# Kernel optimization log

Hardware: AMD Instinct MI355X
Metric: run time of the kernel (lower is better)

## Reference

```python
import jax, jax.numpy as jnp
import numpy as np

FP8_MAX = 448.0


def _quantize_fp8(x):
    """Per-tensor symmetric quantization matching the Triton kernel's decode.

    Encode: u = round(clip(x*scale, -448, 448) / 448 * 127)  (stored as u+128 in uint8)
    Decode: x_hat = u / 127 * 448 / scale,  with scale = 448 / amax(|x|).
    We keep u as a float array of integers in [-127, 127] (the +128 uint8 bias
    cancels in the kernel's `u - 128`).
    """
    amax = jnp.max(jnp.abs(x))
    scale = FP8_MAX / jnp.maximum(amax, jnp.asarray(1e-12, x.dtype))
    q = jnp.clip(x * scale, -FP8_MAX, FP8_MAX)
    u = jnp.round(q / FP8_MAX * 127.0)
    return u, scale


def reference(x, weight):
    orig_shape = x.shape
    K = weight.shape[1]
    x2d = x.reshape(-1, K)                      # [M, K]

    ua, a_scale = _quantize_fp8(x2d)            # codes + per-tensor scale
    uw, w_scale = _quantize_fp8(weight)         # weight: [N, K]

    # Kernel dequant: val = u / 127 * FP8_MAX; acc in fp32; rescale by 1/(a_scale*b_scale)
    a_f = ua * (FP8_MAX / 127.0)
    b_f = (uw * (FP8_MAX / 127.0)).T            # [K, N] (weight_fp8.t())
    acc = a_f @ b_f                              # fp32 accumulate, [M, N]
    out = acc * (1.0 / (a_scale * w_scale))
    out = out.astype(x.dtype)
    return out.reshape(*orig_shape[:-1], weight.shape[0])


def setup_inputs() -> dict:
    key = jax.random.key(0)
    k1, k2 = jax.random.split(key)
    x = jax.random.normal(k1, (4, 2048, 4096), dtype=jnp.float32)
    weight = jax.random.normal(k2, (8192, 4096), dtype=jnp.float32) * 0.02
    return {"x": x, "weight": weight}
```

## Files before the change

### kernel.cpp

```cpp
#include <hip/hip_runtime.h>

#define FP8_MAX_F 448.0f

static constexpr int M = 8192;
static constexpr int N = 8192;
static constexpr int K = 4096;

typedef __attribute__((ext_vector_type(4))) int i32x4;

__global__ void amax_kernel(const float* __restrict__ x, long n4,
                            unsigned* __restrict__ out) {
    unsigned local = 0u;
    const long stride = (long)gridDim.x * blockDim.x;
    const float4* xv = (const float4*)x;
    for (long i = (long)blockIdx.x * blockDim.x + threadIdx.x; i < n4; i += stride) {
        float4 v = xv[i];
        unsigned a0 = __float_as_uint(v.x) & 0x7fffffffu;
        unsigned a1 = __float_as_uint(v.y) & 0x7fffffffu;
        unsigned a2 = __float_as_uint(v.z) & 0x7fffffffu;
        unsigned a3 = __float_as_uint(v.w) & 0x7fffffffu;
        local = max(local, max(max(a0, a1), max(a2, a3)));
    }
    #pragma unroll
    for (int off = 32; off > 0; off >>= 1)
        local = max(local, (unsigned)__shfl_down((int)local, off, 64));
    __shared__ unsigned smax[4];
    if ((threadIdx.x & 63) == 0) smax[threadIdx.x >> 6] = local;
    __syncthreads();
    if (threadIdx.x == 0) {
        unsigned m01 = max(smax[0], smax[1]);
        unsigned m23 = max(smax[2], smax[3]);
        atomicMax(out, max(m01, m23));
    }
}

__global__ void quant_kernel(const float* __restrict__ x, signed char* __restrict__ q,
                             long n16, const unsigned* __restrict__ amax_bits) {
    const float amax = fmaxf(__uint_as_float(*amax_bits), 1e-12f);
    const float s = FP8_MAX_F / amax;
    const long stride = (long)gridDim.x * blockDim.x;
    const float4* xv = (const float4*)x;
    int4* qv = (int4*)q;
    for (long i = (long)blockIdx.x * blockDim.x + threadIdx.x; i < n16; i += stride) {
        signed char c[16];
        #pragma unroll
        for (int j = 0; j < 4; ++j) {
            float4 v = xv[i * 4 + j];
            float e0 = v.x, e1 = v.y, e2 = v.z, e3 = v.w;
            float f0 = fminf(fmaxf(e0 * s, -FP8_MAX_F), FP8_MAX_F);
            float f1 = fminf(fmaxf(e1 * s, -FP8_MAX_F), FP8_MAX_F);
            float f2 = fminf(fmaxf(e2 * s, -FP8_MAX_F), FP8_MAX_F);
            float f3 = fminf(fmaxf(e3 * s, -FP8_MAX_F), FP8_MAX_F);
            c[j * 4 + 0] = (signed char)(int)rintf(f0 / FP8_MAX_F * 127.0f);
            c[j * 4 + 1] = (signed char)(int)rintf(f1 / FP8_MAX_F * 127.0f);
            c[j * 4 + 2] = (signed char)(int)rintf(f2 / FP8_MAX_F * 127.0f);
            c[j * 4 + 3] = (signed char)(int)rintf(f3 / FP8_MAX_F * 127.0f);
        }
        qv[i] = *(const int4*)c;
    }
}

__global__ __launch_bounds__(256) void gemm_i8_kernel(
    const signed char* __restrict__ A, const signed char* __restrict__ B,
    float* __restrict__ C, const unsigned* __restrict__ amax_bits)
{
    __shared__ signed char a_lds[128 * 64];
    __shared__ signed char b_lds[128 * 64];

    const int tid  = threadIdx.x;
    const int wid  = tid >> 6;
    const int lane = tid & 63;

    const long row0 = (long)blockIdx.x * 128;
    const long col0 = (long)blockIdx.y * 128;

    const int wr = (wid >> 1) * 64;
    const int wc = (wid & 1) * 64;

    i32x4 acc[4][4] = {};

    const int srow = lane >> 2;
    const int scol = (lane & 3) * 16;
    const long a_off = (row0 + wid * 16 + srow) * (long)K + scol;
    const long b_off = (col0 + wid * 16 + srow) * (long)K + scol;
    const signed char* aw0 = A + a_off;
    const signed char* aw1 = A + a_off + 64 * (long)K;
    const signed char* bw0 = B + b_off;
    const signed char* bw1 = B + b_off + 64 * (long)K;

    signed char* a_l0 = &a_lds[wid * 1024];
    signed char* a_l1 = &a_lds[4096 + wid * 1024];
    signed char* b_l0 = &b_lds[wid * 1024];
    signed char* b_l1 = &b_lds[4096 + wid * 1024];

    const int fr = lane & 15;
    const int fq = lane >> 4;

    for (int k0 = 0; k0 < K; k0 += 64) {
        __syncthreads();
        __builtin_amdgcn_global_load_lds(
            (const __attribute__((address_space(1))) void*)(aw0 + k0),
            (__attribute__((address_space(3))) void*)a_l0, 16, 0, 0);
        __builtin_amdgcn_global_load_lds(
            (const __attribute__((address_space(1))) void*)(aw1 + k0),
            (__attribute__((address_space(3))) void*)a_l1, 16, 0, 0);
        __builtin_amdgcn_global_load_lds(
            (const __attribute__((address_space(1))) void*)(bw0 + k0),
            (__attribute__((address_space(3))) void*)b_l0, 16, 0, 0);
        __builtin_amdgcn_global_load_lds(
            (const __attribute__((address_space(1))) void*)(bw1 + k0),
            (__attribute__((address_space(3))) void*)b_l1, 16, 0, 0);
        __syncthreads();

        i32x4 af[4], bf[4];
        #pragma unroll
        for (int mi = 0; mi < 4; ++mi)
            af[mi] = *(const i32x4*)&a_lds[(wr + mi * 16 + fr) * 64 + fq * 16];
        #pragma unroll
        for (int ni = 0; ni < 4; ++ni)
            bf[ni] = *(const i32x4*)&b_lds[(wc + ni * 16 + fr) * 64 + fq * 16];

        #pragma unroll
        for (int mi = 0; mi < 4; ++mi)
            #pragma unroll
            for (int ni = 0; ni < 4; ++ni)
                acc[mi][ni] = __builtin_amdgcn_mfma_i32_16x16x64_i8(
                    af[mi], bf[ni], acc[mi][ni], 0, 0, 0);
    }

    const float amax_x = fmaxf(__uint_as_float(amax_bits[0]), 1e-12f);
    const float amax_w = fmaxf(__uint_as_float(amax_bits[1]), 1e-12f);
    const float factor = amax_x * amax_w * (1.0f / (127.0f * 127.0f));

    #pragma unroll
    for (int mi = 0; mi < 4; ++mi) {
        #pragma unroll
        for (int ni = 0; ni < 4; ++ni) {
            const long col = col0 + wc + ni * 16 + fr;
            #pragma unroll
            for (int j = 0; j < 4; ++j) {
                const long row = row0 + wr + mi * 16 + fq * 4 + j;
                C[row * N + col] = (float)acc[mi][ni][j] * factor;
            }
        }
    }
}

extern "C" void kernel_launch(void* const* d_in, const int* in_sizes, int n_in,
                              void* d_out, int out_size, void* d_ws, size_t ws_size,
                              hipStream_t stream) {
    const float* x = (const float*)d_in[0];
    const float* w = (const float*)d_in[1];
    float* out = (float*)d_out;

    unsigned char* ws = (unsigned char*)d_ws;
    unsigned* amax = (unsigned*)ws;
    signed char* aq = (signed char*)(ws + 256);
    signed char* wq = aq + (long)M * K;

    hipMemsetAsync(amax, 0, 2 * sizeof(unsigned), stream);

    const long nx = (long)M * K;
    const long nw = (long)N * K;
    amax_kernel<<<2048, 256, 0, stream>>>(x, nx / 4, &amax[0]);
    amax_kernel<<<2048, 256, 0, stream>>>(w, nw / 4, &amax[1]);
    quant_kernel<<<2048, 256, 0, stream>>>(x, aq, nx / 16, &amax[0]);
    quant_kernel<<<2048, 256, 0, stream>>>(w, wq, nw / 16, &amax[1]);

    dim3 grid(M / 128, N / 128);
    gemm_i8_kernel<<<grid, 256, 0, stream>>>(aq, wq, out, amax);
}
```

Before: 507.3 us.

## Rewrite int8 GEMM with 256x256 tiles, 4-stage LDS pipeline, swizzled layout

The GEMM moves from 128x128 tiles with 4 waves to 256x256 tiles with 8 waves. It uses a four-buffer LDS ring that prefetches two k-steps ahead with direct global-to-LDS loads, and interleaves MFMA phases with s_setprio and explicit barriers. The quantize kernel now writes data in an XOR-swizzled layout that matches the LDS read pattern, to avoid bank conflicts. The amax and quantize kernels for x and weight are each merged into a single launch. In exchange it uses 128KB of LDS per block and many more accumulator registers, with a risk of register spilling or low occupancy.

```diff
diff --git a/kernel.cpp b/kernel.cpp
--- a/kernel.cpp
+++ b/kernel.cpp
@@ -8,138 +8,191 @@
 
 typedef __attribute__((ext_vector_type(4))) int i32x4;
 
-__global__ void amax_kernel(const float* __restrict__ x, long n4,
+#define AS1 __attribute__((address_space(1)))
+#define AS3 __attribute__((address_space(3)))
+#define BARRIER() asm volatile("s_barrier" ::: "memory")
+#define VMCNT(n)  asm volatile("s_waitcnt vmcnt(" #n ")" ::: "memory")
+
+__global__ void amax_kernel(const float* __restrict__ x, const float* __restrict__ w,
                             unsigned* __restrict__ out) {
-    unsigned local = 0u;
+    const long n4x = (long)M * K / 4;
+    const long n4t = n4x + (long)N * K / 4;
+    unsigned lx = 0u, lw = 0u;
     const long stride = (long)gridDim.x * blockDim.x;
-    const float4* xv = (const float4*)x;
-    for (long i = (long)blockIdx.x * blockDim.x + threadIdx.x; i < n4; i += stride) {
-        float4 v = xv[i];
-        unsigned a0 = __float_as_uint(v.x) & 0x7fffffffu;
-        unsigned a1 = __float_as_uint(v.y) & 0x7fffffffu;
-        unsigned a2 = __float_as_uint(v.z) & 0x7fffffffu;
-        unsigned a3 = __float_as_uint(v.w) & 0x7fffffffu;
-        local = max(local, max(max(a0, a1), max(a2, a3)));
+    for (long i = (long)blockIdx.x * blockDim.x + threadIdx.x; i < n4t; i += stride) {
+        if (i < n4x) {
+            float4 v = ((const float4*)x)[i];
+            unsigned a0 = __float_as_uint(v.x) & 0x7fffffffu;
+            unsigned a1 = __float_as_uint(v.y) & 0x7fffffffu;
+            unsigned a2 = __float_as_uint(v.z) & 0x7fffffffu;
+            unsigned a3 = __float_as_uint(v.w) & 0x7fffffffu;
+            lx = max(lx, max(max(a0, a1), max(a2, a3)));
+        } else {
+            float4 v = ((const float4*)w)[i - n4x];
+            unsigned a0 = __float_as_uint(v.x) & 0x7fffffffu;
+            unsigned a1 = __float_as_uint(v.y) & 0x7fffffffu;
+            unsigned a2 = __float_as_uint(v.z) & 0x7fffffffu;
+            unsigned a3 = __float_as_uint(v.w) & 0x7fffffffu;
+            lw = max(lw, max(max(a0, a1), max(a2, a3)));
+        }
     }
     #pragma unroll
-    for (int off = 32; off > 0; off >>= 1)
-        local = max(local, (unsigned)__shfl_down((int)local, off, 64));
-    __shared__ unsigned smax[4];
-    if ((threadIdx.x & 63) == 0) smax[threadIdx.x >> 6] = local;
+    for (int off = 32; off > 0; off >>= 1) {
+        lx = max(lx, (unsigned)__shfl_down((int)lx, off, 64));
+        lw = max(lw, (unsigned)__shfl_down((int)lw, off, 64));
+    }
+    __shared__ unsigned smx[4], smw[4];
+    if ((threadIdx.x & 63) == 0) { smx[threadIdx.x >> 6] = lx; smw[threadIdx.x >> 6] = lw; }
     __syncthreads();
     if (threadIdx.x == 0) {
-        unsigned m01 = max(smax[0], smax[1]);
-        unsigned m23 = max(smax[2], smax[3]);
-        atomicMax(out, max(m01, m23));
-    }
-}
-
-__global__ void quant_kernel(const float* __restrict__ x, signed char* __restrict__ q,
-                             long n16, const unsigned* __restrict__ amax_bits) {
-    const float amax = fmaxf(__uint_as_float(*amax_bits), 1e-12f);
-    const float s = FP8_MAX_F / amax;
+        atomicMax(&out[0], max(max(smx[0], smx[1]), max(smx[2], smx[3])));
+        atomicMax(&out[1], max(max(smw[0], smw[1]), max(smw[2], smw[3])));
+    }
+}
+
+__device__ __forceinline__ signed char quant1(float v, float s) {
+    float f = fminf(fmaxf(v * s, -FP8_MAX_F), FP8_MAX_F);
+    return (signed char)(int)rintf(f / FP8_MAX_F * 127.0f);
+}
+
+__global__ void quant_kernel(const float* __restrict__ x, const float* __restrict__ w,
+                             signed char* __restrict__ qx, signed char* __restrict__ qw,
+                             const unsigned* __restrict__ amax_bits) {
+    const float ax = fmaxf(__uint_as_float(amax_bits[0]), 1e-12f);
+    const float aw = fmaxf(__uint_as_float(amax_bits[1]), 1e-12f);
+    const float sxv = FP8_MAX_F / ax;
+    const float swv = FP8_MAX_F / aw;
+    const long cx = (long)M * K / 16;
+    const long ct = cx + (long)N * K / 16;
     const long stride = (long)gridDim.x * blockDim.x;
-    const float4* xv = (const float4*)x;
-    int4* qv = (int4*)q;
-    for (long i = (long)blockIdx.x * blockDim.x + threadIdx.x; i < n16; i += stride) {
-        signed char c[16];
+    for (long ci = (long)blockIdx.x * blockDim.x + threadIdx.x; ci < ct; ci += stride) {
+        const float* src; signed char* dst; float s; long c;
+        if (ci < cx) { src = x; dst = qx; s = sxv; c = ci; }
+        else         { src = w; dst = qw; s = swv; c = ci - cx; }
+        const long r = c >> 8;
+        const int  cr = (int)(c & 255);
+        const float4* in = (const float4*)(src + r * K + cr * 16);
+        signed char ob[16];
         #pragma unroll
         for (int j = 0; j < 4; ++j) {
-            float4 v = xv[i * 4 + j];
-            float e0 = v.x, e1 = v.y, e2 = v.z, e3 = v.w;
-            float f0 = fminf(fmaxf(e0 * s, -FP8_MAX_F), FP8_MAX_F);
-            float f1 = fminf(fmaxf(e1 * s, -FP8_MAX_F), FP8_MAX_F);
-            float f2 = fminf(fmaxf(e2 * s, -FP8_MAX_F), FP8_MAX_F);
-            float f3 = fminf(fmaxf(e3 * s, -FP8_MAX_F), FP8_MAX_F);
-            c[j * 4 + 0] = (signed char)(int)rintf(f0 / FP8_MAX_F * 127.0f);
-            c[j * 4 + 1] = (signed char)(int)rintf(f1 / FP8_MAX_F * 127.0f);
-            c[j * 4 + 2] = (signed char)(int)rintf(f2 / FP8_MAX_F * 127.0f);
-            c[j * 4 + 3] = (signed char)(int)rintf(f3 / FP8_MAX_F * 127.0f);
+            float4 v = in[j];
+            ob[j * 4 + 0] = quant1(v.x, s);
+            ob[j * 4 + 1] = quant1(v.y, s);
+            ob[j * 4 + 2] = quant1(v.z, s);
+            ob[j * 4 + 3] = quant1(v.w, s);
         }
-        qv[i] = *(const int4*)c;
-    }
-}
-
-__global__ __launch_bounds__(256) void gemm_i8_kernel(
-    const signed char* __restrict__ A, const signed char* __restrict__ B,
+        const int osub = (cr & 3) ^ ((int)(r >> 1) & 3);
+        *(int4*)(dst + r * K + ((long)((cr & ~3) + osub)) * 16) = *(const int4*)ob;
+    }
+}
+
+__global__ __launch_bounds__(512, 2) void gemm_i8_kernel(
+    const signed char* __restrict__ Aq, const signed char* __restrict__ Bq,
     float* __restrict__ C, const unsigned* __restrict__ amax_bits)
 {
-    __shared__ signed char a_lds[128 * 64];
-    __shared__ signed char b_lds[128 * 64];
+    __shared__ signed char lds[4][2][256 * 64];
 
     const int tid  = threadIdx.x;
     const int wid  = tid >> 6;
     const int lane = tid & 63;
-
-    const long row0 = (long)blockIdx.x * 128;
-    const long col0 = (long)blockIdx.y * 128;
-
-    const int wr = (wid >> 1) * 64;
-    const int wc = (wid & 1) * 64;
-
-    i32x4 acc[4][4] = {};
-
-    const int srow = lane >> 2;
-    const int scol = (lane & 3) * 16;
-    const long a_off = (row0 + wid * 16 + srow) * (long)K + scol;
-    const long b_off = (col0 + wid * 16 + srow) * (long)K + scol;
-    const signed char* aw0 = A + a_off;
-    const signed char* aw1 = A + a_off + 64 * (long)K;
-    const signed char* bw0 = B + b_off;
-    const signed char* bw1 = B + b_off + 64 * (long)K;
-
-    signed char* a_l0 = &a_lds[wid * 1024];
-    signed char* a_l1 = &a_lds[4096 + wid * 1024];
-    signed char* b_l0 = &b_lds[wid * 1024];
-    signed char* b_l1 = &b_lds[4096 + wid * 1024];
-
+    const int wm = wid >> 2;
+    const int wn = wid & 3;
     const int fr = lane & 15;
     const int fq = lane >> 4;
 
-    for (int k0 = 0; k0 < K; k0 += 64) {
-        __syncthreads();
-        __builtin_amdgcn_global_load_lds(
-            (const __attribute__((address_space(1))) void*)(aw0 + k0),
-            (__attribute__((address_space(3))) void*)a_l0, 16, 0, 0);
-        __builtin_amdgcn_global_load_lds(
-            (const __attribute__((address_space(1))) void*)(aw1 + k0),
-            (__attribute__((address_space(3))) void*)a_l1, 16, 0, 0);
-        __builtin_amdgcn_global_load_lds(
-            (const __attribute__((address_space(1))) void*)(bw0 + k0),
-            (__attribute__((address_space(3))) void*)b_l0, 16, 0, 0);
-        __builtin_amdgcn_global_load_lds(
-            (const __attribute__((address_space(1))) void*)(bw1 + k0),
-            (__attribute__((address_space(3))) void*)b_l1, 16, 0, 0);
-        __syncthreads();
-
-        i32x4 af[4], bf[4];
-        #pragma unroll
-        for (int mi = 0; mi < 4; ++mi)
-            af[mi] = *(const i32x4*)&a_lds[(wr + mi * 16 + fr) * 64 + fq * 16];
-        #pragma unroll
-        for (int ni = 0; ni < 4; ++ni)
-            bf[ni] = *(const i32x4*)&b_lds[(wc + ni * 16 + fr) * 64 + fq * 16];
-
-        #pragma unroll
-        for (int mi = 0; mi < 4; ++mi)
-            #pragma unroll
-            for (int ni = 0; ni < 4; ++ni)
-                acc[mi][ni] = __builtin_amdgcn_mfma_i32_16x16x64_i8(
-                    af[mi], bf[ni], acc[mi][ni], 0, 0, 0);
-    }
-
-    const float amax_x = fmaxf(__uint_as_float(amax_bits[0]), 1e-12f);
-    const float amax_w = fmaxf(__uint_as_float(amax_bits[1]), 1e-12f);
-    const float factor = amax_x * amax_w * (1.0f / (127.0f * 127.0f));
+    const long row0 = (long)blockIdx.x * 256;
+    const long col0 = (long)blockIdx.y * 256;
+
+    const signed char* Ablk = Aq + row0 * K;
+    const signed char* Bblk = Bq + col0 * K;
+
+    const long stag_off = (long)(tid >> 2) * K + (long)(tid & 3) * 16;
+
+    const int arow = wm * 128 + fr;
+    const int aoff = arow * 64 + ((fq ^ ((arow >> 1) & 3)) * 16);
+    const int brow = wn * 64 + fr;
+    const int boff = brow * 64 + ((fq ^ ((brow >> 1) & 3)) * 16);
+
+    i32x4 acc[8][4] = {};
+
+#define STAGE(gbase, lbase) do { \
+        __builtin_amdgcn_global_load_lds((const AS1 void*)((gbase) + stag_off), \
+            (AS3 void*)((lbase) + wid * 1024), 16, 0, 0); \
+        __builtin_amdgcn_global_load_lds((const AS1 void*)((gbase) + stag_off + 128L * K), \
+            (AS3 void*)((lbase) + 8192 + wid * 1024), 16, 0, 0); \
+    } while (0)
+
+#define MFMA8(nb, bA, bB) do { \
+        _Pragma("unroll") \
+        for (int mi = 0; mi < 8; ++mi) { \
+            acc[mi][nb]     = __builtin_amdgcn_mfma_i32_16x16x64_i8(af[mi], bA, acc[mi][nb], 0, 0, 0); \
+            acc[mi][nb + 1] = __builtin_amdgcn_mfma_i32_16x16x64_i8(af[mi], bB, acc[mi][nb + 1], 0, 0, 0); \
+        } \
+    } while (0)
+
+#define TILE(bufi, STAGE_A_STMT, STAGE_B_STMT, VM_B_STMT) do { \
+        const signed char* la = &lds[bufi][0][0]; \
+        const signed char* lb = &lds[bufi][1][0]; \
+        i32x4 af[8], b0, b1, b2, b3; \
+        STAGE_A_STMT; \
+        _Pragma("unroll") \
+        for (int mi = 0; mi < 8; ++mi) \
+            af[mi] = *(const i32x4*)(la + aoff + mi * 1024); \
+        b0 = *(const i32x4*)(lb + boff + 0 * 1024); \
+        b1 = *(const i32x4*)(lb + boff + 1 * 1024); \
+        BARRIER(); \
+        __builtin_amdgcn_s_setprio(1); \
+        MFMA8(0, b0, b1); \
+        __builtin_amdgcn_s_setprio(0); \
+        BARRIER(); \
+        STAGE_B_STMT; \
+        b2 = *(const i32x4*)(lb + boff + 2 * 1024); \
+        b3 = *(const i32x4*)(lb + boff + 3 * 1024); \
+        VM_B_STMT; \
+        BARRIER(); \
+        __builtin_amdgcn_s_setprio(1); \
+        MFMA8(2, b2, b3); \
+        __builtin_amdgcn_s_setprio(0); \
+        BARRIER(); \
+    } while (0)
+
+    STAGE(Ablk + 0 * 64, &lds[0][0][0]);
+    STAGE(Bblk + 0 * 64, &lds[0][1][0]);
+    STAGE(Ablk + 1 * 64, &lds[1][0][0]);
+    STAGE(Bblk + 1 * 64, &lds[1][1][0]);
+    VMCNT(4);
+    BARRIER();
+
+    #pragma unroll 1
+    for (int t = 0; t <= 60; t += 2) {
+        TILE(t & 3,
+             STAGE(Ablk + (t + 2) * 64, &lds[(t + 2) & 3][0][0]),
+             STAGE(Bblk + (t + 2) * 64, &lds[(t + 2) & 3][1][0]),
+             VMCNT(4));
+        TILE((t + 1) & 3,
+             STAGE(Ablk + (t + 3) * 64, &lds[(t + 3) & 3][0][0]),
+             STAGE(Bblk + (t + 3) * 64, &lds[(t + 3) & 3][1][0]),
+             VMCNT(4));
+    }
+    TILE(2, (void)0, (void)0, VMCNT(0));
+    TILE(3, (void)0, (void)0, (void)0);
+
+#undef TILE
+#undef MFMA8
+#undef STAGE
+
+    const float ax = fmaxf(__uint_as_float(amax_bits[0]), 1e-12f);
+    const float aw = fmaxf(__uint_as_float(amax_bits[1]), 1e-12f);
+    const float factor = ax * aw * (1.0f / (127.0f * 127.0f));
 
     #pragma unroll
-    for (int mi = 0; mi < 4; ++mi) {
+    for (int mi = 0; mi < 8; ++mi) {
         #pragma unroll
         for (int ni = 0; ni < 4; ++ni) {
-            const long col = col0 + wc + ni * 16 + fr;
+            const long col = col0 + wn * 64 + ni * 16 + fr;
             #pragma unroll
             for (int j = 0; j < 4; ++j) {
-                const long row = row0 + wr + mi * 16 + fq * 4 + j;
+                const long row = row0 + wm * 128 + mi * 16 + fq * 4 + j;
                 C[row * N + col] = (float)acc[mi][ni][j] * factor;
             }
         }
@@ -159,14 +212,9 @@
     signed char* wq = aq + (long)M * K;
 
     hipMemsetAsync(amax, 0, 2 * sizeof(unsigned), stream);
-
-    const long nx = (long)M * K;
-    const long nw = (long)N * K;
-    amax_kernel<<<2048, 256, 0, stream>>>(x, nx / 4, &amax[0]);
-    amax_kernel<<<2048, 256, 0, stream>>>(w, nw / 4, &amax[1]);
-    quant_kernel<<<2048, 256, 0, stream>>>(x, aq, nx / 16, &amax[0]);
-    quant_kernel<<<2048, 256, 0, stream>>>(w, wq, nw / 16, &amax[1]);
-
-    dim3 grid(M / 128, N / 128);
-    gemm_i8_kernel<<<grid, 256, 0, stream>>>(aq, wq, out, amax);
-}
+    amax_kernel<<<2048, 256, 0, stream>>>(x, w, amax);
+    quant_kernel<<<4096, 256, 0, stream>>>(x, w, aq, wq, amax);
+
+    dim3 grid(M / 256, N / 256);
+    gemm_i8_kernel<<<grid, 512, 0, stream>>>(aq, wq, out, amax);
+}
```

New measurement: 419.1 us. 1.21x faster.
